# Performance work log

Measured on AMD Instinct MI355X. Metric: run time of the kernel, lower is better.

The kernel has to match this reference:

```python
import jax, jax.numpy as jnp
import numpy as np

B, N, C, H = 2, 2048, 768, 12
HD = C // H  # head dim = 64


def setup_inputs() -> dict:
    key = jax.random.key(0)
    k1, k2, k3 = jax.random.split(key, 3)
    x = jax.random.normal(k1, (B, N, C), dtype=jnp.float32)
    w_qkv = jax.random.normal(k2, (C, 3 * C), dtype=jnp.float32) * (C ** -0.5)
    w_proj = jax.random.normal(k3, (C, C), dtype=jnp.float32) * (C ** -0.5)
    b_proj = jnp.zeros((C,), dtype=jnp.float32)
    return {"x": x, "w_qkv": w_qkv, "w_proj": w_proj, "b_proj": b_proj}


def reference(x, w_qkv, w_proj, b_proj):
    scale = HD ** -0.5
    # qkv projection: [B,N,3C] -> [3,B,H,N,HD]
    qkv = (x @ w_qkv).reshape(B, N, 3, H, HD).transpose(2, 0, 3, 1, 4)
    q, k, v = qkv[0], qkv[1], qkv[2]
    # explicit QK^T softmax V (materializes [B,H,N,N] scores, as in source)
    attn = jnp.einsum("bhqd,bhkd->bhqk", q, k) * scale
    attn = jax.nn.softmax(attn, axis=-1)
    out = jnp.einsum("bhqk,bhkd->bhqd", attn, v)
    out = out.transpose(0, 2, 1, 3).reshape(B, N, C)
    return out @ w_proj + b_proj
```

## Files before the change

### kernel.cpp

```cpp
#include <hip/hip_runtime.h>

#define C_DIM 768
#define NSEQ 2048
#define H_DIM 12
#define HD 64
#define M_ROWS 4096
#define KSPLIT 2
#define PADK 76

typedef float f32x4 __attribute__((ext_vector_type(4)));
typedef short bf16x8 __attribute__((ext_vector_type(8)));
typedef _Float16 f16x8 __attribute__((ext_vector_type(8)));
typedef _Float16 f16x4 __attribute__((ext_vector_type(4)));
typedef __fp16 fp16x2 __attribute__((ext_vector_type(2)));
typedef __fp16 fp16x4 __attribute__((ext_vector_type(4)));
typedef __fp16 fp16x8 __attribute__((ext_vector_type(8)));
typedef unsigned short u16;

#define MFMA_PV(a, b, c) __builtin_amdgcn_mfma_f32_16x16x16f16(a, b, c, 0, 0, 0)

typedef unsigned int __attribute__((address_space(1))) as1_uint;
typedef unsigned int __attribute__((address_space(3))) as3_uint;
__device__ __forceinline__ void dma16(const void* g, void* l) {
  __builtin_amdgcn_global_load_lds((const as1_uint*)g, (as3_uint*)l, 16, 0, 0);
}

__device__ __forceinline__ u16 f2bf(float f) {
  union { float f; unsigned u; } v; v.f = f;
  unsigned u = v.u + 0x7FFFu + ((v.u >> 16) & 1u);
  return (u16)(u >> 16);
}

__global__ __launch_bounds__(256) void prep_kernel(const float* __restrict__ x,
                                                   const float* __restrict__ wq,
                                                   const float* __restrict__ wp,
                                                   u16* __restrict__ x_bf,
                                                   u16* __restrict__ outq,
                                                   __fp16* __restrict__ outp) {
  if (blockIdx.z == 2) {
    const int n4 = M_ROWS * C_DIM / 4;
    int lb = blockIdx.y * 72 + blockIdx.x;
    int i0 = lb * 256 + threadIdx.x;
    {
      float4 v = ((const float4*)x)[i0];
      ushort4 o;
      o.x = f2bf(v.x); o.y = f2bf(v.y); o.z = f2bf(v.z); o.w = f2bf(v.w);
      ((ushort4*)x_bf)[i0] = o;
    }
    int i1 = i0 + 442368;
    if (i1 < n4) {
      float4 v = ((const float4*)x)[i1];
      ushort4 o;
      o.x = f2bf(v.x); o.y = f2bf(v.y); o.z = f2bf(v.z); o.w = f2bf(v.w);
      ((ushort4*)x_bf)[i1] = o;
    }
    return;
  }
  const int R = C_DIM;
  __shared__ float t[32][33];
  int tx = threadIdx.x & 31, ty = threadIdx.x >> 5;
  int c0 = blockIdx.x * 32, r0 = blockIdx.y * 32;
  if (blockIdx.z == 0) {
    const int Cc = 3 * C_DIM;
#pragma unroll
    for (int i = 0; i < 4; i++)
      t[ty + i * 8][tx] = wq[(size_t)(r0 + ty + i * 8) * Cc + c0 + tx];
    __syncthreads();
#pragma unroll
    for (int i = 0; i < 4; i++)
      outq[(size_t)(c0 + ty + i * 8) * R + r0 + tx] = f2bf(t[tx][ty + i * 8]);
  } else {
    if (blockIdx.x >= 24) return;
    const int Cc = C_DIM;
#pragma unroll
    for (int i = 0; i < 4; i++)
      t[ty + i * 8][tx] = wp[(size_t)(r0 + ty + i * 8) * Cc + c0 + tx];
    __syncthreads();
#pragma unroll
    for (int i = 0; i < 4; i++)
      outp[(size_t)(c0 + ty + i * 8) * R + r0 + tx] = (__fp16)t[tx][ty + i * 8];
  }
}

__device__ __forceinline__ void gemm_core_128_db(const u16* __restrict__ A,
                                                 const u16* __restrict__ BT,
                                                 int m0, int n0,
                                                 u16 (*la)[128 * 32], u16 (*lb)[128 * 32],
                                                 f32x4 acc[4][4]) {
  const int K = C_DIM;
  int tid = threadIdx.x, lane = tid & 63, wave = tid >> 6;
  int wm = (wave >> 1) * 64, wn = (wave & 1) * 64;
  int quad = lane >> 4, l16 = lane & 15;

  int r0 = wave * 16 + (lane >> 2);
  int sw = (((lane & 3) ^ (r0 & 3)) * 8);
  const u16* ga0 = A + (size_t)(m0 + r0) * K + sw;
  const u16* ga1 = A + (size_t)(m0 + r0 + 64) * K + sw;
  const u16* gb0 = BT + (size_t)(n0 + r0) * K + sw;
  const u16* gb1 = BT + (size_t)(n0 + r0 + 64) * K + sw;
  int ofs0 = wave * 16 * 32, ofs1 = ofs0 + 64 * 32;

  dma16(ga0, la[0] + ofs0);
  dma16(ga1, la[0] + ofs1);
  dma16(gb0, lb[0] + ofs0);
  dma16(gb1, lb[0] + ofs1);

  const int NT = K / 32;
  for (int kt = 0; kt < NT; kt++) {
    int cur = kt & 1, nxt = cur ^ 1;
    __syncthreads();
    if (kt < NT - 1) {
      int k0 = (kt + 1) * 32;
      dma16(ga0 + k0, la[nxt] + ofs0);
      dma16(ga1 + k0, la[nxt] + ofs1);
      dma16(gb0 + k0, lb[nxt] + ofs0);
      dma16(gb1 + k0, lb[nxt] + ofs1);
    }
    bf16x8 af[4], bfr[4];
#pragma unroll
    for (int mt = 0; mt < 4; mt++) {
      int r = wm + mt * 16 + l16;
      af[mt] = *(const bf16x8*)(la[cur] + r * 32 + ((quad ^ (r & 3)) * 8));
    }
#pragma unroll
    for (int nt = 0; nt < 4; nt++) {
      int r = wn + nt * 16 + l16;
      bfr[nt] = *(const bf16x8*)(lb[cur] + r * 32 + ((quad ^ (r & 3)) * 8));
    }
#pragma unroll
    for (int mt = 0; mt < 4; mt++)
#pragma unroll
      for (int nt = 0; nt < 4; nt++)
        acc[mt][nt] = __builtin_amdgcn_mfma_f32_16x16x32_bf16(bfr[nt], af[mt], acc[mt][nt], 0, 0, 0);
  }
}

#define Q_PRESCALE 0.18033688011112042f
__global__ __launch_bounds__(256) void gemm_qkv_kernel(const u16* __restrict__ A,
                                                       const u16* __restrict__ BT,
                                                       _Float16* __restrict__ qb,
                                                       _Float16* __restrict__ kb,
                                                       _Float16* __restrict__ vtb) {
  __shared__ __align__(16) u16 la[2][128 * 32];
  __shared__ __align__(16) u16 lb[2][128 * 32];
  f32x4 acc[4][4] = {};
  int m0 = blockIdx.x * 128, n0 = blockIdx.y * 128;
  gemm_core_128_db(A, BT, m0, n0, la, lb, acc);

  int lane = threadIdx.x & 63, wave = threadIdx.x >> 6;
  int wm = (wave >> 1) * 64, wn = (wave & 1) * 64;
  int quad = lane >> 4, l16 = lane & 15;
#pragma unroll
  for (int mt = 0; mt < 4; mt++) {
#pragma unroll
    for (int nt = 0; nt < 4; nt++) {
      int gm = m0 + wm + mt * 16 + l16;
      int b = gm >> 11, n = gm & 2047;
      int gn0 = n0 + wn + nt * 16 + quad * 4;
      int which = gn0 / C_DIM;
      int cc = gn0 - which * C_DIM;
      int h = cc >> 6, d0 = cc & 63;
      size_t bh = (size_t)(b * H_DIM + h);
      if (which == 2) {
#pragma unroll
        for (int r = 0; r < 4; r++)
          vtb[(bh * HD + d0 + r) * NSEQ + n] = (_Float16)acc[mt][nt][r];
      } else if (which == 0) {
        f16x4 hv;
#pragma unroll
        for (int r = 0; r < 4; r++) hv[r] = (_Float16)(acc[mt][nt][r] * Q_PRESCALE);
        *(f16x4*)(qb + (bh * NSEQ + n) * HD + d0) = hv;
      } else {
        f16x4 hv;
#pragma unroll
        for (int r = 0; r < 4; r++) hv[r] = (_Float16)acc[mt][nt][r];
        *(f16x4*)(kb + (bh * NSEQ + n) * HD + d0) = hv;
      }
    }
  }
}

__global__ __launch_bounds__(256) void gemm_proj_kernel(const __fp16* __restrict__ opart,
                                                        const float* __restrict__ lpart,
                                                        const u16* __restrict__ BT,
                                                        const float* __restrict__ bias,
                                                        float* __restrict__ out) {
  __shared__ __align__(16) u16 la[2][64 * 32];
  __shared__ __align__(16) u16 lb[2][128 * 32];
  int tid = threadIdx.x, lane = tid & 63, wave = tid >> 6;
  int quad = lane >> 4, l16 = lane & 15;
  int wm = (wave >> 1) * 32, wn = (wave & 1) * 64;
  int m0 = blockIdx.x * 64, n0 = blockIdx.y * 128;

  int r0 = wave * 16 + (lane >> 2);
  int swb = (((lane & 3) ^ (r0 & 3)) * 8);
  const u16* gb0 = BT + (size_t)(n0 + r0) * C_DIM + swb;
  const u16* gb1 = BT + (size_t)(n0 + r0 + 64) * C_DIM + swb;
  int ofsB0 = wave * 16 * 32, ofsB1 = ofsB0 + 64 * 32;

  int ar = r0, cj = lane & 3;
  int m = m0 + ar;
  int bb = m >> 11, q = m & 2047;
  const __fp16* ap = opart + (size_t)m * C_DIM + cj * 8;
  int wslotA = ar * 32 + ((cj ^ (ar & 3)) * 8);

  f32x4 acc[2][4] = {};
  union pk_t { fp16x2 h2[4]; uint4 v; };

#define COMBINE_A(dstbuf, k0, hh)                                              \
  {                                                                            \
    float fs[8] = {0, 0, 0, 0, 0, 0, 0, 0};                                    \
    float l = 0.f;                                                             \
    _Pragma("unroll") for (int kk = 0; kk < KSPLIT; kk++) {                    \
      fp16x8 pv = *(const fp16x8*)(ap + (size_t)kk * M_ROWS * C_DIM + (k0));   \
      _Pragma("unroll") for (int j = 0; j < 8; j++) fs[j] += (float)pv[j];     \
      l += lpart[((size_t)kk * H_DIM * 2 + bb * H_DIM + (hh)) * NSEQ + q];     \
    }                                                                          \
    float inv = 1.f / l;                                                       \
    pk_t w;                                                                    \
    _Pragma("unroll") for (int j = 0; j < 4; j++)                              \
        w.h2[j] = __builtin_amdgcn_cvt_pkrtz(fs[2 * j] * inv, fs[2 * j + 1] * inv); \
    *(uint4*)(la[dstbuf] + wslotA) = w.v;                                      \
  }

  dma16(gb0, lb[0] + ofsB0);
  dma16(gb1, lb[0] + ofsB1);
  COMBINE_A(0, 0, 0);

  const int NT = C_DIM / 32;
  for (int kt = 0; kt < NT; kt++) {
    int cur = kt & 1, nxt = cur ^ 1;
    __syncthreads();
    if (kt < NT - 1) {
      int k0 = (kt + 1) * 32;
      dma16(gb0 + k0, lb[nxt] + ofsB0);
      dma16(gb1 + k0, lb[nxt] + ofsB1);
      COMBINE_A(nxt, k0, (kt + 1) >> 1);
    }
    f16x8 af[2], bf[4];
#pragma unroll
    for (int mt = 0; mt < 2; mt++) {
      int r = wm + mt * 16 + l16;
      af[mt] = *(const f16x8*)(la[cur] + r * 32 + ((quad ^ (r & 3)) * 8));
    }
#pragma unroll
    for (int nt = 0; nt < 4; nt++) {
      int r = wn + nt * 16 + l16;
      bf[nt] = *(const f16x8*)(lb[cur] + r * 32 + ((quad ^ (r & 3)) * 8));
    }
#pragma unroll
    for (int mt = 0; mt < 2; mt++)
#pragma unroll
      for (int nt = 0; nt < 4; nt++)
        acc[mt][nt] = __builtin_amdgcn_mfma_f32_16x16x32_f16(bf[nt], af[mt], acc[mt][nt], 0, 0, 0);
  }

#pragma unroll
  for (int mt = 0; mt < 2; mt++) {
#pragma unroll
    for (int nt = 0; nt < 4; nt++) {
      int gm = m0 + wm + mt * 16 + l16;
      int gn0 = n0 + wn + nt * 16 + quad * 4;
      float4 bv = *(const float4*)(bias + gn0);
      float4 o4;
      o4.x = acc[mt][nt][0] + bv.x;
      o4.y = acc[mt][nt][1] + bv.y;
      o4.z = acc[mt][nt][2] + bv.z;
      o4.w = acc[mt][nt][3] + bv.w;
      *(float4*)(out + (size_t)gm * C_DIM + gn0) = o4;
    }
  }
}

__global__ __launch_bounds__(256) void attn_kernel(const _Float16* __restrict__ qb,
                                                   const _Float16* __restrict__ kb,
                                                   const _Float16* __restrict__ vtb,
                                                   __fp16* __restrict__ opart,
                                                   float* __restrict__ lpart) {
  __shared__ __align__(16) u16 lk[2][64 * PADK];
  __shared__ __align__(16) u16 lv[2][64 * PADK];
  int bh = blockIdx.y, qblk = blockIdx.x, ks = blockIdx.z;
  int tid = threadIdx.x, lane = tid & 63, wave = tid >> 6;
  int quad = lane >> 4, l16 = lane & 15;

  const _Float16* q_bh = qb + (size_t)bh * NSEQ * HD;
  const u16* k_bh = (const u16*)(kb + (size_t)bh * NSEQ * HD);
  const u16* v_bh = (const u16*)(vtb + (size_t)bh * HD * NSEQ);

  int q0 = qblk * 128 + wave * 32 + l16;
  f16x8 qf[2][2];
#pragma unroll
  for (int qt = 0; qt < 2; qt++) {
    const _Float16* qp = q_bh + (size_t)(q0 + qt * 16) * HD + quad * 8;
    qf[qt][0] = *(const f16x8*)qp;
    qf[qt][1] = *(const f16x8*)(qp + 32);
  }

  f32x4 o[2][4] = {};
  float l_i[2] = {0.f, 0.f};

  int srow = tid >> 3, scj = tid & 7;
  const u16* kp0 = k_bh + (size_t)srow * HD + scj * 8;
  const u16* kp1 = kp0 + (size_t)32 * HD;
  const u16* vp0 = v_bh + (size_t)srow * NSEQ + scj * 8;
  const u16* vp1 = vp0 + (size_t)32 * NSEQ;
  int w0 = srow * PADK + scj * 8, w1 = (srow + 32) * PADK + scj * 8;

  const int kt_beg = ks * (NSEQ / 64 / KSPLIT);
  const int kt_end = kt_beg + (NSEQ / 64 / KSPLIT);

  {
    int k0 = kt_beg * 64;
    *(uint4*)(lk[0] + w0) = *(const uint4*)(kp0 + (size_t)k0 * HD);
    *(uint4*)(lk[0] + w1) = *(const uint4*)(kp1 + (size_t)k0 * HD);
    *(uint4*)(lv[0] + w0) = *(const uint4*)(vp0 + k0);
    *(uint4*)(lv[0] + w1) = *(const uint4*)(vp1 + k0);
  }

  for (int kt = kt_beg; kt < kt_end; kt++) {
    int cur = kt & 1, nxt = cur ^ 1;
    __syncthreads();

    uint4 rk0, rk1, rv0, rv1;
    if (kt < kt_end - 1) {
      int k0 = (kt + 1) * 64;
      rk0 = *(const uint4*)(kp0 + (size_t)k0 * HD);
      rk1 = *(const uint4*)(kp1 + (size_t)k0 * HD);
      rv0 = *(const uint4*)(vp0 + k0);
      rv1 = *(const uint4*)(vp1 + k0);
    }

    f32x4 s0[4], s1[4];
#pragma unroll
    for (int nt = 0; nt < 4; nt++) {
      const u16* kp = lk[cur] + (nt * 16 + l16) * PADK + quad * 8;
      f16x8 kf0 = *(const f16x8*)kp;
      f16x8 kf1 = *(const f16x8*)(kp + 32);
      f32x4 t0 = {}, t1 = {};
      t0 = __builtin_amdgcn_mfma_f32_16x16x32_f16(kf0, qf[0][0], t0, 0, 0, 0);
      t0 = __builtin_amdgcn_mfma_f32_16x16x32_f16(kf1, qf[0][1], t0, 0, 0, 0);
      t1 = __builtin_amdgcn_mfma_f32_16x16x32_f16(kf0, qf[1][0], t1, 0, 0, 0);
      t1 = __builtin_amdgcn_mfma_f32_16x16x32_f16(kf1, qf[1][1], t1, 0, 0, 0);
      s0[nt] = t0; s1[nt] = t1;
    }

#pragma unroll
    for (int nt = 0; nt < 4; nt++) {
      float a0 = __builtin_amdgcn_exp2f(s0[nt][0]);
      float a1 = __builtin_amdgcn_exp2f(s0[nt][1]);
      float a2 = __builtin_amdgcn_exp2f(s0[nt][2]);
      float a3 = __builtin_amdgcn_exp2f(s0[nt][3]);
      l_i[0] += (a0 + a1) + (a2 + a3);
      float b0 = __builtin_amdgcn_exp2f(s1[nt][0]);
      float b1 = __builtin_amdgcn_exp2f(s1[nt][1]);
      float b2 = __builtin_amdgcn_exp2f(s1[nt][2]);
      float b3 = __builtin_amdgcn_exp2f(s1[nt][3]);
      l_i[1] += (b0 + b1) + (b2 + b3);
      union { fp16x2 h2[2]; f16x4 h4; } pa, pb;
      pa.h2[0] = __builtin_amdgcn_cvt_pkrtz(a0, a1);
      pa.h2[1] = __builtin_amdgcn_cvt_pkrtz(a2, a3);
      pb.h2[0] = __builtin_amdgcn_cvt_pkrtz(b0, b1);
      pb.h2[1] = __builtin_amdgcn_cvt_pkrtz(b2, b3);
#pragma unroll
      for (int dt = 0; dt < 4; dt++) {
        f16x4 vf = *(const f16x4*)(lv[cur] + (dt * 16 + l16) * PADK + nt * 16 + quad * 4);
        o[0][dt] = MFMA_PV(vf, pa.h4, o[0][dt]);
        o[1][dt] = MFMA_PV(vf, pb.h4, o[1][dt]);
      }
    }

    if (kt < kt_end - 1) {
      *(uint4*)(lk[nxt] + w0) = rk0;
      *(uint4*)(lk[nxt] + w1) = rk1;
      *(uint4*)(lv[nxt] + w0) = rv0;
      *(uint4*)(lv[nxt] + w1) = rv1;
    }
  }

#pragma unroll
  for (int qt = 0; qt < 2; qt++) {
    l_i[qt] += __shfl_xor(l_i[qt], 16);
    l_i[qt] += __shfl_xor(l_i[qt], 32);
  }

  int b = bh / H_DIM, h = bh % H_DIM;
  __fp16* obase = opart + (size_t)ks * M_ROWS * C_DIM;
  float* lrow = lpart + ((size_t)ks * H_DIM * 2 + bh) * NSEQ;
#pragma unroll
  for (int qt = 0; qt < 2; qt++) {
    int q = q0 + qt * 16;
    if (quad == 0) lrow[q] = l_i[qt];
    __fp16* orow = obase + (size_t)(b * NSEQ + q) * C_DIM + h * HD;
#pragma unroll
    for (int dt = 0; dt < 4; dt++) {
      union { fp16x2 h2[2]; fp16x4 h4; } ov;
      ov.h2[0] = __builtin_amdgcn_cvt_pkrtz(o[qt][dt][0], o[qt][dt][1]);
      ov.h2[1] = __builtin_amdgcn_cvt_pkrtz(o[qt][dt][2], o[qt][dt][3]);
      *(fp16x4*)(orow + dt * 16 + quad * 4) = ov.h4;
    }
  }
}

extern "C" void kernel_launch(void* const* d_in, const int* in_sizes, int n_in,
                              void* d_out, int out_size, void* d_ws, size_t ws_size,
                              hipStream_t stream) {
  const float* x = (const float*)d_in[0];
  const float* w_qkv = (const float*)d_in[1];
  const float* w_proj = (const float*)d_in[2];
  const float* b_proj = (const float*)d_in[3];
  float* out = (float*)d_out;

  char* ws = (char*)d_ws;
  u16* x_bf        = (u16*)(ws);
  u16* wqkvT       = (u16*)(ws + 6291456);
  __fp16* wprojT   = (__fp16*)(ws + 9830400);
  _Float16* qb     = (_Float16*)(ws + 11010048);
  _Float16* kb     = (_Float16*)(ws + 17301504);
  _Float16* vtb    = (_Float16*)(ws + 23592960);
  __fp16* opart    = (__fp16*)(ws + 29884416);
  float* lpart     = (float*)(ws + 42467328);

  prep_kernel<<<dim3(72, 24, 3), 256, 0, stream>>>(x, w_qkv, w_proj, x_bf, wqkvT, wprojT);
  gemm_qkv_kernel<<<dim3(32, 18), 256, 0, stream>>>(x_bf, wqkvT, qb, kb, vtb);
  attn_kernel<<<dim3(16, 24, KSPLIT), 256, 0, stream>>>(qb, kb, vtb, opart, lpart);
  gemm_proj_kernel<<<dim3(64, 6), 256, 0, stream>>>(opart, lpart, (const u16*)wprojT,
                                                    b_proj, out);
}
```

Measured before the change: 191.3 us.

## Enlarge attention query tile, XOR-swizzle LDS, and raise key split to four

```diff
diff --git a/kernel.cpp b/kernel.cpp
--- a/kernel.cpp
+++ b/kernel.cpp
@@ -5,8 +5,7 @@
 #define H_DIM 12
 #define HD 64
 #define M_ROWS 4096
-#define KSPLIT 2
-#define PADK 76
+#define KSPLIT 4
 
 typedef float f32x4 __attribute__((ext_vector_type(4)));
 typedef short bf16x8 __attribute__((ext_vector_type(8)));
@@ -277,8 +276,8 @@
                                                    const _Float16* __restrict__ vtb,
                                                    __fp16* __restrict__ opart,
                                                    float* __restrict__ lpart) {
-  __shared__ __align__(16) u16 lk[2][64 * PADK];
-  __shared__ __align__(16) u16 lv[2][64 * PADK];
+  __shared__ __align__(16) u16 lk[2][64 * 64];
+  __shared__ __align__(16) u16 lv[2][64 * 64];
   int bh = blockIdx.y, qblk = blockIdx.x, ks = blockIdx.z;
   int tid = threadIdx.x, lane = tid & 63, wave = tid >> 6;
   int quad = lane >> 4, l16 = lane & 15;
@@ -287,24 +286,25 @@
   const u16* k_bh = (const u16*)(kb + (size_t)bh * NSEQ * HD);
   const u16* v_bh = (const u16*)(vtb + (size_t)bh * HD * NSEQ);
 
-  int q0 = qblk * 128 + wave * 32 + l16;
-  f16x8 qf[2][2];
-#pragma unroll
-  for (int qt = 0; qt < 2; qt++) {
+  int q0 = qblk * 256 + wave * 64 + l16;
+  f16x8 qf[4][2];
+#pragma unroll
+  for (int qt = 0; qt < 4; qt++) {
     const _Float16* qp = q_bh + (size_t)(q0 + qt * 16) * HD + quad * 8;
     qf[qt][0] = *(const f16x8*)qp;
     qf[qt][1] = *(const f16x8*)(qp + 32);
   }
 
-  f32x4 o[2][4] = {};
-  float l_i[2] = {0.f, 0.f};
+  f32x4 o[4][4] = {};
+  float l_i[4] = {0.f, 0.f, 0.f, 0.f};
 
   int srow = tid >> 3, scj = tid & 7;
   const u16* kp0 = k_bh + (size_t)srow * HD + scj * 8;
   const u16* kp1 = kp0 + (size_t)32 * HD;
   const u16* vp0 = v_bh + (size_t)srow * NSEQ + scj * 8;
   const u16* vp1 = vp0 + (size_t)32 * NSEQ;
-  int w0 = srow * PADK + scj * 8, w1 = (srow + 32) * PADK + scj * 8;
+  int slot = (scj ^ (srow & 7)) * 8;
+  int w0 = srow * 64 + slot, w1 = (srow + 32) * 64 + slot;
 
   const int kt_beg = ks * (NSEQ / 64 / KSPLIT);
   const int kt_end = kt_beg + (NSEQ / 64 / KSPLIT);
@@ -330,42 +330,41 @@
       rv1 = *(const uint4*)(vp1 + k0);
     }
 
-    f32x4 s0[4], s1[4];
+    int rs = l16 & 7;
 #pragma unroll
     for (int nt = 0; nt < 4; nt++) {
-      const u16* kp = lk[cur] + (nt * 16 + l16) * PADK + quad * 8;
-      f16x8 kf0 = *(const f16x8*)kp;
-      f16x8 kf1 = *(const f16x8*)(kp + 32);
-      f32x4 t0 = {}, t1 = {};
-      t0 = __builtin_amdgcn_mfma_f32_16x16x32_f16(kf0, qf[0][0], t0, 0, 0, 0);
-      t0 = __builtin_amdgcn_mfma_f32_16x16x32_f16(kf1, qf[0][1], t0, 0, 0, 0);
-      t1 = __builtin_amdgcn_mfma_f32_16x16x32_f16(kf0, qf[1][0], t1, 0, 0, 0);
-      t1 = __builtin_amdgcn_mfma_f32_16x16x32_f16(kf1, qf[1][1], t1, 0, 0, 0);
-      s0[nt] = t0; s1[nt] = t1;
-    }
-
-#pragma unroll
-    for (int nt = 0; nt < 4; nt++) {
-      float a0 = __builtin_amdgcn_exp2f(s0[nt][0]);
-      float a1 = __builtin_amdgcn_exp2f(s0[nt][1]);
-      float a2 = __builtin_amdgcn_exp2f(s0[nt][2]);
-      float a3 = __builtin_amdgcn_exp2f(s0[nt][3]);
-      l_i[0] += (a0 + a1) + (a2 + a3);
-      float b0 = __builtin_amdgcn_exp2f(s1[nt][0]);
-      float b1 = __builtin_amdgcn_exp2f(s1[nt][1]);
-      float b2 = __builtin_amdgcn_exp2f(s1[nt][2]);
-      float b3 = __builtin_amdgcn_exp2f(s1[nt][3]);
-      l_i[1] += (b0 + b1) + (b2 + b3);
-      union { fp16x2 h2[2]; f16x4 h4; } pa, pb;
-      pa.h2[0] = __builtin_amdgcn_cvt_pkrtz(a0, a1);
-      pa.h2[1] = __builtin_amdgcn_cvt_pkrtz(a2, a3);
-      pb.h2[0] = __builtin_amdgcn_cvt_pkrtz(b0, b1);
-      pb.h2[1] = __builtin_amdgcn_cvt_pkrtz(b2, b3);
+      const u16* kbp = lk[cur] + (nt * 16 + l16) * 64;
+      f16x8 kf0 = *(const f16x8*)(kbp + ((quad ^ rs) * 8));
+      f16x8 kf1 = *(const f16x8*)(kbp + (((quad + 4) ^ rs) * 8));
+      f32x4 s[4];
+#pragma unroll
+      for (int qt = 0; qt < 4; qt++) {
+        f32x4 t = {};
+        t = __builtin_amdgcn_mfma_f32_16x16x32_f16(kf0, qf[qt][0], t, 0, 0, 0);
+        t = __builtin_amdgcn_mfma_f32_16x16x32_f16(kf1, qf[qt][1], t, 0, 0, 0);
+        s[qt] = t;
+      }
+      f16x4 p[4];
+#pragma unroll
+      for (int qt = 0; qt < 4; qt++) {
+        float e0 = __builtin_amdgcn_exp2f(s[qt][0]);
+        float e1 = __builtin_amdgcn_exp2f(s[qt][1]);
+        float e2 = __builtin_amdgcn_exp2f(s[qt][2]);
+        float e3 = __builtin_amdgcn_exp2f(s[qt][3]);
+        l_i[qt] += (e0 + e1) + (e2 + e3);
+        union { fp16x2 h2[2]; f16x4 h4; } u;
+        u.h2[0] = __builtin_amdgcn_cvt_pkrtz(e0, e1);
+        u.h2[1] = __builtin_amdgcn_cvt_pkrtz(e2, e3);
+        p[qt] = u.h4;
+      }
 #pragma unroll
       for (int dt = 0; dt < 4; dt++) {
-        f16x4 vf = *(const f16x4*)(lv[cur] + (dt * 16 + l16) * PADK + nt * 16 + quad * 4);
-        o[0][dt] = MFMA_PV(vf, pa.h4, o[0][dt]);
-        o[1][dt] = MFMA_PV(vf, pb.h4, o[1][dt]);
+        int c = nt * 2 + (quad >> 1);
+        f16x4 vf = *(const f16x4*)(lv[cur] + (dt * 16 + l16) * 64 +
+                                   ((c ^ rs) * 8) + (quad & 1) * 4);
+#pragma unroll
+        for (int qt = 0; qt < 4; qt++)
+          o[qt][dt] = MFMA_PV(vf, p[qt], o[qt][dt]);
       }
     }
 
@@ -378,7 +377,7 @@
   }
 
 #pragma unroll
-  for (int qt = 0; qt < 2; qt++) {
+  for (int qt = 0; qt < 4; qt++) {
     l_i[qt] += __shfl_xor(l_i[qt], 16);
     l_i[qt] += __shfl_xor(l_i[qt], 32);
   }
@@ -387,7 +386,7 @@
   __fp16* obase = opart + (size_t)ks * M_ROWS * C_DIM;
   float* lrow = lpart + ((size_t)ks * H_DIM * 2 + bh) * NSEQ;
 #pragma unroll
-  for (int qt = 0; qt < 2; qt++) {
+  for (int qt = 0; qt < 4; qt++) {
     int q = q0 + qt * 16;
     if (quad == 0) lrow[q] = l_i[qt];
     __fp16* orow = obase + (size_t)(b * NSEQ + q) * C_DIM + h * HD;
@@ -418,11 +417,11 @@
   _Float16* kb     = (_Float16*)(ws + 17301504);
   _Float16* vtb    = (_Float16*)(ws + 23592960);
   __fp16* opart    = (__fp16*)(ws + 29884416);
-  float* lpart     = (float*)(ws + 42467328);
+  float* lpart     = (float*)(ws + 55050240);
 
   prep_kernel<<<dim3(72, 24, 3), 256, 0, stream>>>(x, w_qkv, w_proj, x_bf, wqkvT, wprojT);
   gemm_qkv_kernel<<<dim3(32, 18), 256, 0, stream>>>(x_bf, wqkvT, qb, kb, vtb);
-  attn_kernel<<<dim3(16, 24, KSPLIT), 256, 0, stream>>>(qb, kb, vtb, opart, lpart);
+  attn_kernel<<<dim3(8, 24, KSPLIT), 256, 0, stream>>>(qb, kb, vtb, opart, lpart);
   gemm_proj_kernel<<<dim3(64, 6), 256, 0, stream>>>(opart, lpart, (const u16*)wprojT,
                                                     b_proj, out);
 }
```

Result: faster. 184.8 us (-3.4%).
